# Kernel tuning notes

Hardware: AMD Instinct MI355X
Metric: run time of the kernel (lower is better)

Reference implementation:

```python
import jax, jax.numpy as jnp
import numpy as np

EMB = 1024
HEADS = 16
B, N = 2, 2048

def setup_inputs() -> dict:
    key = jax.random.key(0)
    ks = jax.random.split(key, 9)
    s = 1.0 / np.sqrt(EMB)
    return {
        "x": jax.random.normal(ks[0], (B, N, EMB), dtype=jnp.float32),
        "Wq": jax.random.normal(ks[1], (EMB, EMB), dtype=jnp.float32) * s,
        "bq": jax.random.normal(ks[2], (EMB,), dtype=jnp.float32) * 0.01,
        "Wk": jax.random.normal(ks[3], (EMB, EMB), dtype=jnp.float32) * s,
        "bk": jax.random.normal(ks[4], (EMB,), dtype=jnp.float32) * 0.01,
        "Wv": jax.random.normal(ks[5], (EMB, EMB), dtype=jnp.float32) * s,
        "bv": jax.random.normal(ks[6], (EMB,), dtype=jnp.float32) * 0.01,
        "Wo": jax.random.normal(ks[7], (EMB, EMB), dtype=jnp.float32) * s,
        "bo": jax.random.normal(ks[8], (EMB,), dtype=jnp.float32) * 0.01,
    }

def _split_heads(t):
    b, n, e = t.shape
    return t.reshape(b, n, HEADS, e // HEADS).transpose(0, 2, 1, 3)  # b h n d

def reference(x, Wq, bq, Wk, bk, Wv, bv, Wo, bo):
    q = _split_heads(x @ Wq + bq)
    k = _split_heads(x @ Wk + bk)
    v = _split_heads(x @ Wv + bv)
    # NOTE: original scales by sqrt(emb_size), not sqrt(head_dim)
    scaling = jnp.asarray(EMB, x.dtype) ** 0.5
    energy = jnp.einsum('bhqd,bhkd->bhqk', q, k)
    att = jax.nn.softmax(energy / scaling, axis=-1)
    out = jnp.einsum('bhqk,bhkd->bhqd', att, v)
    out = out.transpose(0, 2, 1, 3).reshape(x.shape[0], x.shape[1], EMB)
    return out @ Wo + bo
```

## Files before the change

### kernel.cpp

```cpp
#include <hip/hip_runtime.h>
#include <hip/hip_bf16.h>

typedef __bf16 bf16_t;
typedef bf16_t bf16x8 __attribute__((ext_vector_type(8)));
typedef float f32x4 __attribute__((ext_vector_type(4)));
typedef float f32x16 __attribute__((ext_vector_type(16)));

#define EMB 1024
#define HEADS 16
#define BATCH 2
#define SEQ 2048
#define HD 64
#define TOKENS (BATCH * SEQ)

__device__ __forceinline__ void gld16(bf16_t* lds_dst, const bf16_t* g_src) {
    __builtin_amdgcn_global_load_lds(
        (const __attribute__((address_space(1))) unsigned int*)g_src,
        (__attribute__((address_space(3))) unsigned int*)lds_dst, 16, 0, 0);
}

__device__ __forceinline__ unsigned cvt_pk_bf16(float lo, float hi) {
    unsigned r;
    asm("v_cvt_pk_bf16_f32 %0, %1, %2" : "=v"(r) : "v"(lo), "v"(hi));
    return r;
}

__device__ __forceinline__ float exp2_fast(float x) {
#if __has_builtin(__builtin_amdgcn_exp2f)
    return __builtin_amdgcn_exp2f(x);
#else
    return __expf(x * 0.69314718056f);
#endif
}

__global__ __launch_bounds__(256) void convert_x(const float* __restrict__ x,
                                                 bf16_t* __restrict__ xb) {
    size_t i = ((size_t)blockIdx.x * 256 + threadIdx.x) * 16;
    f32x4 v0 = *(const f32x4*)&x[i];
    f32x4 v1 = *(const f32x4*)&x[i + 4];
    f32x4 v2 = *(const f32x4*)&x[i + 8];
    f32x4 v3 = *(const f32x4*)&x[i + 12];
    bf16x8 o0, o1;
#pragma unroll
    for (int j = 0; j < 4; ++j) {
        o0[j] = (bf16_t)v0[j]; o0[4 + j] = (bf16_t)v1[j];
        o1[j] = (bf16_t)v2[j]; o1[4 + j] = (bf16_t)v3[j];
    }
    *(bf16x8*)&xb[i] = o0;
    *(bf16x8*)&xb[i + 8] = o1;
}

__global__ __launch_bounds__(256) void prep_w(
    const float* __restrict__ W0, const float* __restrict__ W1,
    const float* __restrict__ W2, const float* __restrict__ W3,
    bf16_t* __restrict__ T0, bf16_t* __restrict__ T1,
    bf16_t* __restrict__ T2, bf16_t* __restrict__ T3) {
    __shared__ __align__(16) bf16_t T[64][72];
    int z = blockIdx.z;
    const float* src = (z == 0) ? W0 : (z == 1) ? W1 : (z == 2) ? W2 : W3;
    bf16_t* dst = (z == 0) ? T0 : (z == 1) ? T1 : (z == 2) ? T2 : T3;
    int k0 = blockIdx.y * 64, n0 = blockIdx.x * 64;
    int r = threadIdx.x >> 2, c4 = (threadIdx.x & 3) * 16;
    f32x4 v[4];
#pragma unroll
    for (int q = 0; q < 4; ++q)
        v[q] = *(const f32x4*)&src[(size_t)(k0 + r) * 1024 + n0 + c4 + q * 4];
#pragma unroll
    for (int j = 0; j < 16; ++j) T[c4 + j][r] = (bf16_t)v[j >> 2][j & 3];
    __syncthreads();
    bf16x8 o0 = *(const bf16x8*)&T[r][c4];
    bf16x8 o1 = *(const bf16x8*)&T[r][c4 + 8];
    *(bf16x8*)&dst[(size_t)(n0 + r) * 1024 + k0 + c4] = o0;
    *(bf16x8*)&dst[(size_t)(n0 + r) * 1024 + k0 + c4 + 8] = o1;
}

__global__ __launch_bounds__(256) void vtrans(const bf16_t* __restrict__ V,
                                              bf16_t* __restrict__ Vt) {
    __shared__ __align__(16) bf16_t T[64][72];
    int bh = blockIdx.y, n0 = blockIdx.x * 64;
    int r = threadIdx.x >> 2, c4 = (threadIdx.x & 3) * 16;
    const bf16_t* src = &V[((size_t)bh * SEQ + n0 + r) * HD + c4];
    bf16x8 v0 = *(const bf16x8*)&src[0];
    bf16x8 v1 = *(const bf16x8*)&src[8];
#pragma unroll
    for (int j = 0; j < 8; ++j) { T[c4 + j][r] = v0[j]; T[c4 + 8 + j][r] = v1[j]; }
    __syncthreads();
    bf16x8 o0 = *(const bf16x8*)&T[r][c4];
    bf16x8 o1 = *(const bf16x8*)&T[r][c4 + 8];
    bf16_t* dst = &Vt[((size_t)bh * HD + r) * SEQ + n0 + c4];
    *(bf16x8*)&dst[0] = o0;
    *(bf16x8*)&dst[8] = o1;
}

template <typename TO>
__global__ __launch_bounds__(256) void gemm128(
    const bf16_t* __restrict__ A,
    const bf16_t* __restrict__ Wt0, const bf16_t* __restrict__ Wt1, const bf16_t* __restrict__ Wt2,
    const float* __restrict__ b0, const float* __restrict__ b1, const float* __restrict__ b2,
    TO* __restrict__ o0, TO* __restrict__ o1, TO* __restrict__ o2,
    int md0, int md1, int md2, float sc0, float sc1, float sc2) {
    __shared__ __align__(16) bf16_t As[2][128 * 32];
    __shared__ __align__(16) bf16_t Bs[2][128 * 32];

    const int tid = threadIdx.x, w = tid >> 6, lane = tid & 63;
    const int quad = lane >> 4, c = lane & 15;
    const int wm = (w >> 1) * 64, wn = (w & 1) * 64;

    const int nx = blockIdx.y & 7, ny = blockIdx.x * 4 + (blockIdx.y >> 3);
    const int m0 = ny * 128, n0 = nx * 128;

    const int z = blockIdx.z;
    const bf16_t* W = (z == 0) ? Wt0 : (z == 1) ? Wt1 : Wt2;
    const float* bias = (z == 0) ? b0 : (z == 1) ? b1 : b2;
    TO* out = (z == 0) ? o0 : (z == 1) ? o1 : o2;
    const int mode = (z == 0) ? md0 : (z == 1) ? md1 : md2;
    const float scale = (z == 0) ? sc0 : (z == 1) ? sc1 : sc2;

    f32x4 acc[4][4];
#pragma unroll
    for (int i = 0; i < 4; ++i)
#pragma unroll
        for (int j = 0; j < 4; ++j) acc[i][j] = (f32x4){0.f, 0.f, 0.f, 0.f};

    const int srow = lane >> 2, schunk = lane & 3;
    const bf16_t* Ag = A + (size_t)m0 * 1024;
    const bf16_t* Bg = W + (size_t)n0 * 1024;

    int gsrc[2], ldst[2];
#pragma unroll
    for (int s = 0; s < 2; ++s) {
        int rg = (w * 2 + s) * 16;
        gsrc[s] = (rg + srow) * 1024 + schunk * 8;
        ldst[s] = rg * 32;
    }

#pragma unroll
    for (int s = 0; s < 2; ++s) {
        gld16(&As[0][ldst[s]], &Ag[gsrc[s]]);
        gld16(&Bs[0][ldst[s]], &Bg[gsrc[s]]);
    }
    __syncthreads();

#define GEMM_STEP(TT, CUR)                                                     \
    {                                                                          \
        if ((TT) + 1 < 32) {                                                   \
            int kn = ((TT) + 1) * 32;                                          \
            _Pragma("unroll")                                                  \
            for (int s = 0; s < 2; ++s) {                                      \
                gld16(&As[(CUR) ^ 1][ldst[s]], &Ag[gsrc[s] + kn]);             \
                gld16(&Bs[(CUR) ^ 1][ldst[s]], &Bg[gsrc[s] + kn]);             \
            }                                                                  \
        }                                                                      \
        bf16x8 af[4], bfv[4];                                                  \
        _Pragma("unroll")                                                      \
        for (int t = 0; t < 4; ++t)                                            \
            af[t] = *(const bf16x8*)&As[CUR][(wm + t * 16 + c) * 32 + quad * 8]; \
        _Pragma("unroll")                                                      \
        for (int t = 0; t < 4; ++t)                                            \
            bfv[t] = *(const bf16x8*)&Bs[CUR][(wn + t * 16 + c) * 32 + quad * 8]; \
        __builtin_amdgcn_s_setprio(1);                                         \
        _Pragma("unroll")                                                      \
        for (int mt = 0; mt < 4; ++mt)                                         \
            _Pragma("unroll")                                                  \
            for (int nt = 0; nt < 4; ++nt)                                     \
                acc[mt][nt] = __builtin_amdgcn_mfma_f32_16x16x32_bf16(         \
                    af[mt], bfv[nt], acc[mt][nt], 0, 0, 0);                    \
        __builtin_amdgcn_s_setprio(0);                                         \
        __syncthreads();                                                       \
    }

    for (int t = 0; t < 32; t += 2) {
        GEMM_STEP(t, 0)
        GEMM_STEP(t + 1, 1)
    }
#undef GEMM_STEP

#pragma unroll
    for (int nt = 0; nt < 4; ++nt) {
        int col = n0 + wn + nt * 16 + c;
        float bv = bias[col];
#pragma unroll
        for (int mt = 0; mt < 4; ++mt)
#pragma unroll
            for (int r = 0; r < 4; ++r) {
                int row = m0 + wm + mt * 16 + quad * 4 + r;
                float v = (acc[mt][nt][r] + bv) * scale;
                size_t idx;
                if (mode == 0) {
                    idx = (size_t)row * 1024 + col;
                } else {
                    int bb = row >> 11, n = row & 2047;
                    int hh = col >> 6, d = col & 63;
                    idx = ((size_t)(bb * HEADS + hh) * SEQ + n) * HD + d;
                }
                out[idx] = (TO)v;
            }
    }
}

__global__ __launch_bounds__(256) void attn_kernel(
    const bf16_t* __restrict__ Q, const bf16_t* __restrict__ K,
    const bf16_t* __restrict__ Vt, bf16_t* __restrict__ O) {
    __shared__ __align__(16) bf16_t Qs[128 * 64];
    __shared__ __align__(16) bf16_t Ks[2][64 * 64];
    __shared__ __align__(16) bf16_t Vs[2][64 * 64];

    const int tid = threadIdx.x, w = tid >> 6, lane = tid & 63;
    const int hi = lane >> 5, lq = lane & 31;

    const int lin = blockIdx.x + (blockIdx.y << 4);
    const int xcd = lin & 7, slot = lin >> 3;
    const int bh = xcd + ((slot >> 4) << 3);
    const int q0 = (slot & 15) << 7;
    const int b = bh >> 4, h = bh & 15;

    const int srow8 = lane >> 3, sch = lane & 7;

    const bf16_t* Qg = Q + ((size_t)bh * SEQ + q0) * HD;
    const bf16_t* Kg0 = K + (size_t)bh * SEQ * HD;
    const bf16_t* Vg0 = Vt + (size_t)bh * HD * SEQ;

    int sl[2], sgK[2], sgV[2];
#pragma unroll
    for (int s = 0; s < 2; ++s) {
        int rg = (w * 2 + s) * 8;
        int row = rg + srow8;
        int g = sch ^ (row & 7);
        sl[s] = rg * 64;
        sgK[s] = row * 64 + g * 8;
        sgV[s] = row * SEQ + g * 8;
    }
    int rd[4];
#pragma unroll
    for (int dc = 0; dc < 4; ++dc)
        rd[dc] = lq * 64 + (((dc * 2 + hi) ^ (lq & 7)) * 8);

#pragma unroll
    for (int s = 0; s < 4; ++s) {
        int rg = (w * 4 + s) * 8;
        int row = rg + srow8;
        int g = sch ^ (row & 7);
        gld16(&Qs[rg * 64], &Qg[(size_t)row * 64 + g * 8]);
    }
#pragma unroll
    for (int s = 0; s < 2; ++s) {
        gld16(&Ks[0][sl[s]], &Kg0[sgK[s]]);
        gld16(&Vs[0][sl[s]], &Vg0[sgV[s]]);
    }
    __syncthreads();

    bf16x8 qf[4];
#pragma unroll
    for (int dc = 0; dc < 4; ++dc)
        qf[dc] = *(const bf16x8*)&Qs[w * 2048 + rd[dc]];

    f32x16 Oacc0, Oacc1;
#pragma unroll
    for (int r = 0; r < 16; ++r) { Oacc0[r] = 0.f; Oacc1[r] = 0.f; }
    float lp = 0.f;

    const bf16_t* KgN = Kg0 + 64 * HD;
    const bf16_t* VgN = Vg0 + 64;

#define ATTN_STEP(TT, CUR)                                                     \
    {                                                                          \
        if ((TT) + 1 < SEQ / 64) {                                             \
            _Pragma("unroll")                                                  \
            for (int s = 0; s < 2; ++s) {                                      \
                gld16(&Ks[(CUR) ^ 1][sl[s]], &KgN[sgK[s]]);                    \
                gld16(&Vs[(CUR) ^ 1][sl[s]], &VgN[sgV[s]]);                    \
            }                                                                  \
            KgN += 64 * HD; VgN += 64;                                         \
        }                                                                      \
        f32x16 St0, St1;                                                       \
        _Pragma("unroll")                                                      \
        for (int r = 0; r < 16; ++r) { St0[r] = 0.f; St1[r] = 0.f; }           \
        __builtin_amdgcn_s_setprio(1);                                         \
        _Pragma("unroll")                                                      \
        for (int dc = 0; dc < 4; ++dc) {                                       \
            bf16x8 k0 = *(const bf16x8*)&Ks[CUR][rd[dc]];                      \
            bf16x8 k1 = *(const bf16x8*)&Ks[CUR][rd[dc] + 2048];               \
            St0 = __builtin_amdgcn_mfma_f32_32x32x16_bf16(k0, qf[dc], St0, 0, 0, 0); \
            St1 = __builtin_amdgcn_mfma_f32_32x32x16_bf16(k1, qf[dc], St1, 0, 0, 0); \
        }                                                                      \
        __builtin_amdgcn_s_setprio(0);                                         \
        _Pragma("unroll")                                                      \
        for (int r = 0; r < 16; ++r) {                                         \
            St0[r] = exp2_fast(St0[r]); lp += St0[r];                          \
            St1[r] = exp2_fast(St1[r]); lp += St1[r];                          \
        }                                                                      \
        bf16x8 pf[4];                                                          \
        PACKFRAG(St0, 0, 0) PACKFRAG(St0, 1, 1)                                \
        PACKFRAG(St1, 0, 2) PACKFRAG(St1, 1, 3)                                \
        __builtin_amdgcn_s_setprio(1);                                         \
        _Pragma("unroll")                                                      \
        for (int f = 0; f < 4; ++f) {                                          \
            bf16x8 v0 = *(const bf16x8*)&Vs[CUR][rd[f]];                       \
            bf16x8 v1 = *(const bf16x8*)&Vs[CUR][rd[f] + 2048];                \
            Oacc0 = __builtin_amdgcn_mfma_f32_32x32x16_bf16(pf[f], v0, Oacc0, 0, 0, 0); \
            Oacc1 = __builtin_amdgcn_mfma_f32_32x32x16_bf16(pf[f], v1, Oacc1, 0, 0, 0); \
        }                                                                      \
        __builtin_amdgcn_s_setprio(0);                                         \
        __syncthreads();                                                       \
    }

#define PACKFRAG(SS, c2, dstIdx)                                               \
        {                                                                      \
            unsigned pa = cvt_pk_bf16(SS[8 * (c2) + 0], SS[8 * (c2) + 1]);     \
            unsigned pb = cvt_pk_bf16(SS[8 * (c2) + 4], SS[8 * (c2) + 5]);     \
            unsigned pc = cvt_pk_bf16(SS[8 * (c2) + 2], SS[8 * (c2) + 3]);     \
            unsigned pd = cvt_pk_bf16(SS[8 * (c2) + 6], SS[8 * (c2) + 7]);     \
            asm volatile("v_permlane32_swap_b32 %0, %1" : "+v"(pa), "+v"(pb)); \
            asm volatile("v_permlane32_swap_b32 %0, %1" : "+v"(pc), "+v"(pd)); \
            union { unsigned u[4]; bf16x8 v; } pu;                             \
            pu.u[0] = pa; pu.u[1] = pc; pu.u[2] = pb; pu.u[3] = pd;            \
            pf[dstIdx] = pu.v;                                                 \
        }

    for (int t = 0; t < SEQ / 64; t += 2) {
        ATTN_STEP(t, 0)
        ATTN_STEP(t + 1, 1)
    }
#undef ATTN_STEP
#undef PACKFRAG

    lp += __shfl_xor(lp, 32);
    float rl = 1.0f / lp;

#pragma unroll
    for (int r = 0; r < 16; ++r) {
        int q_loc = (r & 3) + 8 * (r >> 2) + 4 * hi;
        float rr = __shfl(rl, q_loc);
        int qrow = q0 + w * 32 + q_loc;
        size_t base = ((size_t)(b * SEQ + qrow)) * EMB + h * 64;
        O[base + lq] = (bf16_t)(Oacc0[r] * rr);
        O[base + 32 + lq] = (bf16_t)(Oacc1[r] * rr);
    }
}

extern "C" void kernel_launch(void* const* d_in, const int* in_sizes, int n_in,
                              void* d_out, int out_size, void* d_ws, size_t ws_size,
                              hipStream_t stream) {
    (void)in_sizes; (void)n_in; (void)out_size; (void)ws_size;
    const float* x  = (const float*)d_in[0];
    const float* Wq = (const float*)d_in[1];
    const float* bq = (const float*)d_in[2];
    const float* Wk = (const float*)d_in[3];
    const float* bk = (const float*)d_in[4];
    const float* Wv = (const float*)d_in[5];
    const float* bv = (const float*)d_in[6];
    const float* Wo = (const float*)d_in[7];
    const float* bo = (const float*)d_in[8];

    bf16_t* ws = (bf16_t*)d_ws;
    const size_t NELEM = (size_t)TOKENS * EMB;
    const size_t WELEM = (size_t)EMB * EMB;
    bf16_t* Qb  = ws;
    bf16_t* Kb  = ws + NELEM;
    bf16_t* Vb  = ws + 2 * NELEM;
    bf16_t* Ob  = ws + 3 * NELEM;
    bf16_t* xb  = ws + 4 * NELEM;
    bf16_t* Vtb = xb;
    bf16_t* Wt0 = ws + 5 * NELEM;
    bf16_t* Wt1 = Wt0 + WELEM;
    bf16_t* Wt2 = Wt0 + 2 * WELEM;
    bf16_t* Wt3 = Wt0 + 3 * WELEM;

    hipLaunchKernelGGL(convert_x, dim3(1024), dim3(256), 0, stream, x, xb);
    hipLaunchKernelGGL(prep_w, dim3(16, 16, 4), dim3(256), 0, stream,
                       Wq, Wk, Wv, Wo, Wt0, Wt1, Wt2, Wt3);
    hipLaunchKernelGGL((gemm128<bf16_t>), dim3(8, 32, 3), dim3(256), 0, stream,
                       xb, Wt0, Wt1, Wt2, bq, bk, bv, Qb, Kb, Vb,
                       1, 1, 1, 0.0450842204f, 1.0f, 1.0f);
    hipLaunchKernelGGL(vtrans, dim3(32, 32), dim3(256), 0, stream, Vb, Vtb);
    hipLaunchKernelGGL(attn_kernel, dim3(16, 32), dim3(256), 0, stream, Qb, Kb, Vtb, Ob);
    hipLaunchKernelGGL((gemm128<float>), dim3(8, 32, 1), dim3(256), 0, stream,
                       Ob, Wt3, Wt3, Wt3, bo, bo, bo,
                       (float*)d_out, (float*)d_out, (float*)d_out,
                       0, 0, 0, 1.0f, 1.0f, 1.0f);
}
```

Measured before the change: 215.7 us.

## Triple-buffer GEMM and attention loads, fuse V transpose into QKV epilogue

Both the projection GEMM and the attention kernel move from double to triple-buffered LDS staging. Each step waits on a vmcnt counter and issues a raw barrier, which replaces a full __syncthreads after every step and lets two tiles be in flight during compute. The QKV GEMM epilogue gains a mode that writes V directly in transposed head layout with packed 4-element stores, removing the separate vtrans kernel launch and its extra memory pass. The cost is more LDS per block, which may reduce occupancy, and hand-tuned waitcnt values whose correctness depends on the number of outstanding loads.

```diff
diff --git a/kernel.cpp b/kernel.cpp
--- a/kernel.cpp
+++ b/kernel.cpp
@@ -32,6 +32,9 @@
     return __expf(x * 0.69314718056f);
 #endif
 }
+
+#define WAITV(N) asm volatile("s_waitcnt vmcnt(" #N ")" ::: "memory")
+#define BAR() __builtin_amdgcn_s_barrier()
 
 __global__ __launch_bounds__(256) void convert_x(const float* __restrict__ x,
                                                  bf16_t* __restrict__ xb) {
@@ -74,24 +77,6 @@
     *(bf16x8*)&dst[(size_t)(n0 + r) * 1024 + k0 + c4 + 8] = o1;
 }
 
-__global__ __launch_bounds__(256) void vtrans(const bf16_t* __restrict__ V,
-                                              bf16_t* __restrict__ Vt) {
-    __shared__ __align__(16) bf16_t T[64][72];
-    int bh = blockIdx.y, n0 = blockIdx.x * 64;
-    int r = threadIdx.x >> 2, c4 = (threadIdx.x & 3) * 16;
-    const bf16_t* src = &V[((size_t)bh * SEQ + n0 + r) * HD + c4];
-    bf16x8 v0 = *(const bf16x8*)&src[0];
-    bf16x8 v1 = *(const bf16x8*)&src[8];
-#pragma unroll
-    for (int j = 0; j < 8; ++j) { T[c4 + j][r] = v0[j]; T[c4 + 8 + j][r] = v1[j]; }
-    __syncthreads();
-    bf16x8 o0 = *(const bf16x8*)&T[r][c4];
-    bf16x8 o1 = *(const bf16x8*)&T[r][c4 + 8];
-    bf16_t* dst = &Vt[((size_t)bh * HD + r) * SEQ + n0 + c4];
-    *(bf16x8*)&dst[0] = o0;
-    *(bf16x8*)&dst[8] = o1;
-}
-
 template <typename TO>
 __global__ __launch_bounds__(256) void gemm128(
     const bf16_t* __restrict__ A,
@@ -99,8 +84,8 @@
     const float* __restrict__ b0, const float* __restrict__ b1, const float* __restrict__ b2,
     TO* __restrict__ o0, TO* __restrict__ o1, TO* __restrict__ o2,
     int md0, int md1, int md2, float sc0, float sc1, float sc2) {
-    __shared__ __align__(16) bf16_t As[2][128 * 32];
-    __shared__ __align__(16) bf16_t Bs[2][128 * 32];
+    __shared__ __align__(16) bf16_t As[3][128 * 32];
+    __shared__ __align__(16) bf16_t Bs[3][128 * 32];
 
     const int tid = threadIdx.x, w = tid >> 6, lane = tid & 63;
     const int quad = lane >> 4, c = lane & 15;
@@ -139,25 +124,21 @@
         gld16(&As[0][ldst[s]], &Ag[gsrc[s]]);
         gld16(&Bs[0][ldst[s]], &Bg[gsrc[s]]);
     }
-    __syncthreads();
-
-#define GEMM_STEP(TT, CUR)                                                     \
+#pragma unroll
+    for (int s = 0; s < 2; ++s) {
+        gld16(&As[1][ldst[s]], &Ag[gsrc[s] + 32]);
+        gld16(&Bs[1][ldst[s]], &Bg[gsrc[s] + 32]);
+    }
+
+#define GFRAGS(CUR)                                                            \
     {                                                                          \
-        if ((TT) + 1 < 32) {                                                   \
-            int kn = ((TT) + 1) * 32;                                          \
-            _Pragma("unroll")                                                  \
-            for (int s = 0; s < 2; ++s) {                                      \
-                gld16(&As[(CUR) ^ 1][ldst[s]], &Ag[gsrc[s] + kn]);             \
-                gld16(&Bs[(CUR) ^ 1][ldst[s]], &Bg[gsrc[s] + kn]);             \
-            }                                                                  \
-        }                                                                      \
         bf16x8 af[4], bfv[4];                                                  \
         _Pragma("unroll")                                                      \
-        for (int t = 0; t < 4; ++t)                                            \
-            af[t] = *(const bf16x8*)&As[CUR][(wm + t * 16 + c) * 32 + quad * 8]; \
-        _Pragma("unroll")                                                      \
-        for (int t = 0; t < 4; ++t)                                            \
-            bfv[t] = *(const bf16x8*)&Bs[CUR][(wn + t * 16 + c) * 32 + quad * 8]; \
+        for (int t2 = 0; t2 < 4; ++t2)                                         \
+            af[t2] = *(const bf16x8*)&As[CUR][(wm + t2 * 16 + c) * 32 + quad * 8]; \
+        _Pragma("unroll")                                                      \
+        for (int t2 = 0; t2 < 4; ++t2)                                         \
+            bfv[t2] = *(const bf16x8*)&Bs[CUR][(wn + t2 * 16 + c) * 32 + quad * 8]; \
         __builtin_amdgcn_s_setprio(1);                                         \
         _Pragma("unroll")                                                      \
         for (int mt = 0; mt < 4; ++mt)                                         \
@@ -166,35 +147,64 @@
                 acc[mt][nt] = __builtin_amdgcn_mfma_f32_16x16x32_bf16(         \
                     af[mt], bfv[nt], acc[mt][nt], 0, 0, 0);                    \
         __builtin_amdgcn_s_setprio(0);                                         \
-        __syncthreads();                                                       \
-    }
-
-    for (int t = 0; t < 32; t += 2) {
-        GEMM_STEP(t, 0)
-        GEMM_STEP(t + 1, 1)
-    }
-#undef GEMM_STEP
-
+    }
+
+#define GSTEP(T, CUR)                                                          \
+    {                                                                          \
+        WAITV(4);                                                              \
+        BAR();                                                                 \
+        int kn = ((T) + 2) * 32;                                               \
+        _Pragma("unroll")                                                      \
+        for (int s = 0; s < 2; ++s) {                                          \
+            gld16(&As[((CUR) + 2) % 3][ldst[s]], &Ag[gsrc[s] + kn]);           \
+            gld16(&Bs[((CUR) + 2) % 3][ldst[s]], &Bg[gsrc[s] + kn]);           \
+        }                                                                      \
+        GFRAGS(CUR)                                                            \
+    }
+
+    for (int t = 0; t < 30; t += 3) {
+        GSTEP(t, 0)
+        GSTEP(t + 1, 1)
+        GSTEP(t + 2, 2)
+    }
+    WAITV(4); BAR(); GFRAGS(0)
+    WAITV(0); BAR(); GFRAGS(1)
+#undef GSTEP
+#undef GFRAGS
+
+    typedef TO TOx4 __attribute__((ext_vector_type(4)));
 #pragma unroll
     for (int nt = 0; nt < 4; ++nt) {
         int col = n0 + wn + nt * 16 + c;
         float bv = bias[col];
 #pragma unroll
-        for (int mt = 0; mt < 4; ++mt)
-#pragma unroll
-            for (int r = 0; r < 4; ++r) {
-                int row = m0 + wm + mt * 16 + quad * 4 + r;
-                float v = (acc[mt][nt][r] + bv) * scale;
-                size_t idx;
-                if (mode == 0) {
-                    idx = (size_t)row * 1024 + col;
-                } else {
-                    int bb = row >> 11, n = row & 2047;
-                    int hh = col >> 6, d = col & 63;
-                    idx = ((size_t)(bb * HEADS + hh) * SEQ + n) * HD + d;
+        for (int mt = 0; mt < 4; ++mt) {
+            if (mode == 2) {
+                int row = m0 + wm + mt * 16 + quad * 4;
+                int bb = row >> 11, n = row & 2047;
+                int hh = col >> 6, d = col & 63;
+                TOx4 pk;
+#pragma unroll
+                for (int r = 0; r < 4; ++r)
+                    pk[r] = (TO)((acc[mt][nt][r] + bv) * scale);
+                *(TOx4*)&out[((size_t)(bb * HEADS + hh) * HD + d) * SEQ + n] = pk;
+            } else {
+#pragma unroll
+                for (int r = 0; r < 4; ++r) {
+                    int row = m0 + wm + mt * 16 + quad * 4 + r;
+                    float v = (acc[mt][nt][r] + bv) * scale;
+                    size_t idx;
+                    if (mode == 0) {
+                        idx = (size_t)row * 1024 + col;
+                    } else {
+                        int bb = row >> 11, n = row & 2047;
+                        int hh = col >> 6, d = col & 63;
+                        idx = ((size_t)(bb * HEADS + hh) * SEQ + n) * HD + d;
+                    }
+                    out[idx] = (TO)v;
                 }
-                out[idx] = (TO)v;
             }
+        }
     }
 }
 
@@ -202,8 +212,8 @@
     const bf16_t* __restrict__ Q, const bf16_t* __restrict__ K,
     const bf16_t* __restrict__ Vt, bf16_t* __restrict__ O) {
     __shared__ __align__(16) bf16_t Qs[128 * 64];
-    __shared__ __align__(16) bf16_t Ks[2][64 * 64];
-    __shared__ __align__(16) bf16_t Vs[2][64 * 64];
+    __shared__ __align__(16) bf16_t Ks[3][64 * 64];
+    __shared__ __align__(16) bf16_t Vs[3][64 * 64];
 
     const int tid = threadIdx.x, w = tid >> 6, lane = tid & 63;
     const int hi = lane >> 5, lq = lane & 31;
@@ -247,8 +257,14 @@
         gld16(&Ks[0][sl[s]], &Kg0[sgK[s]]);
         gld16(&Vs[0][sl[s]], &Vg0[sgV[s]]);
     }
-    __syncthreads();
-
+#pragma unroll
+    for (int s = 0; s < 2; ++s) {
+        gld16(&Ks[1][sl[s]], &Kg0[64 * HD + sgK[s]]);
+        gld16(&Vs[1][sl[s]], &Vg0[64 + sgV[s]]);
+    }
+
+    WAITV(8);
+    BAR();
     bf16x8 qf[4];
 #pragma unroll
     for (int dc = 0; dc < 4; ++dc)
@@ -259,50 +275,8 @@
     for (int r = 0; r < 16; ++r) { Oacc0[r] = 0.f; Oacc1[r] = 0.f; }
     float lp = 0.f;
 
-    const bf16_t* KgN = Kg0 + 64 * HD;
-    const bf16_t* VgN = Vg0 + 64;
-
-#define ATTN_STEP(TT, CUR)                                                     \
-    {                                                                          \
-        if ((TT) + 1 < SEQ / 64) {                                             \
-            _Pragma("unroll")                                                  \
-            for (int s = 0; s < 2; ++s) {                                      \
-                gld16(&Ks[(CUR) ^ 1][sl[s]], &KgN[sgK[s]]);                    \
-                gld16(&Vs[(CUR) ^ 1][sl[s]], &VgN[sgV[s]]);                    \
-            }                                                                  \
-            KgN += 64 * HD; VgN += 64;                                         \
-        }                                                                      \
-        f32x16 St0, St1;                                                       \
-        _Pragma("unroll")                                                      \
-        for (int r = 0; r < 16; ++r) { St0[r] = 0.f; St1[r] = 0.f; }           \
-        __builtin_amdgcn_s_setprio(1);                                         \
-        _Pragma("unroll")                                                      \
-        for (int dc = 0; dc < 4; ++dc) {                                       \
-            bf16x8 k0 = *(const bf16x8*)&Ks[CUR][rd[dc]];                      \
-            bf16x8 k1 = *(const bf16x8*)&Ks[CUR][rd[dc] + 2048];               \
-            St0 = __builtin_amdgcn_mfma_f32_32x32x16_bf16(k0, qf[dc], St0, 0, 0, 0); \
-            St1 = __builtin_amdgcn_mfma_f32_32x32x16_bf16(k1, qf[dc], St1, 0, 0, 0); \
-        }                                                                      \
-        __builtin_amdgcn_s_setprio(0);                                         \
-        _Pragma("unroll")                                                      \
-        for (int r = 0; r < 16; ++r) {                                         \
-            St0[r] = exp2_fast(St0[r]); lp += St0[r];                          \
-            St1[r] = exp2_fast(St1[r]); lp += St1[r];                          \
-        }                                                                      \
-        bf16x8 pf[4];                                                          \
-        PACKFRAG(St0, 0, 0) PACKFRAG(St0, 1, 1)                                \
-        PACKFRAG(St1, 0, 2) PACKFRAG(St1, 1, 3)                                \
-        __builtin_amdgcn_s_setprio(1);                                         \
-        _Pragma("unroll")                                                      \
-        for (int f = 0; f < 4; ++f) {                                          \
-            bf16x8 v0 = *(const bf16x8*)&Vs[CUR][rd[f]];                       \
-            bf16x8 v1 = *(const bf16x8*)&Vs[CUR][rd[f] + 2048];                \
-            Oacc0 = __builtin_amdgcn_mfma_f32_32x32x16_bf16(pf[f], v0, Oacc0, 0, 0, 0); \
-            Oacc1 = __builtin_amdgcn_mfma_f32_32x32x16_bf16(pf[f], v1, Oacc1, 0, 0, 0); \
-        }                                                                      \
-        __builtin_amdgcn_s_setprio(0);                                         \
-        __syncthreads();                                                       \
-    }
+    const bf16_t* KgN = Kg0 + 2 * 64 * HD;
+    const bf16_t* VgN = Vg0 + 2 * 64;
 
 #define PACKFRAG(SS, c2, dstIdx)                                               \
         {                                                                      \
@@ -317,11 +291,59 @@
             pf[dstIdx] = pu.v;                                                 \
         }
 
-    for (int t = 0; t < SEQ / 64; t += 2) {
-        ATTN_STEP(t, 0)
-        ATTN_STEP(t + 1, 1)
-    }
-#undef ATTN_STEP
+#define ACORE(CUR)                                                             \
+    {                                                                          \
+        f32x16 St0, St1;                                                       \
+        _Pragma("unroll")                                                      \
+        for (int r = 0; r < 16; ++r) { St0[r] = 0.f; St1[r] = 0.f; }           \
+        __builtin_amdgcn_s_setprio(1);                                         \
+        _Pragma("unroll")                                                      \
+        for (int dc = 0; dc < 4; ++dc) {                                       \
+            bf16x8 k0 = *(const bf16x8*)&Ks[CUR][rd[dc]];                      \
+            bf16x8 k1 = *(const bf16x8*)&Ks[CUR][rd[dc] + 2048];               \
+            St0 = __builtin_amdgcn_mfma_f32_32x32x16_bf16(k0, qf[dc], St0, 0, 0, 0); \
+            St1 = __builtin_amdgcn_mfma_f32_32x32x16_bf16(k1, qf[dc], St1, 0, 0, 0); \
+        }                                                                      \
+        __builtin_amdgcn_s_setprio(0);                                         \
+        _Pragma("unroll")                                                      \
+        for (int r = 0; r < 16; ++r) {                                         \
+            St0[r] = exp2_fast(St0[r]); lp += St0[r];                          \
+            St1[r] = exp2_fast(St1[r]); lp += St1[r];                          \
+        }                                                                      \
+        bf16x8 pf[4];                                                          \
+        PACKFRAG(St0, 0, 0) PACKFRAG(St0, 1, 1)                                \
+        PACKFRAG(St1, 0, 2) PACKFRAG(St1, 1, 3)                                \
+        __builtin_amdgcn_s_setprio(1);                                         \
+        _Pragma("unroll")                                                      \
+        for (int f = 0; f < 4; ++f) {                                          \
+            bf16x8 v0 = *(const bf16x8*)&Vs[CUR][rd[f]];                       \
+            bf16x8 v1 = *(const bf16x8*)&Vs[CUR][rd[f] + 2048];                \
+            Oacc0 = __builtin_amdgcn_mfma_f32_32x32x16_bf16(pf[f], v0, Oacc0, 0, 0, 0); \
+            Oacc1 = __builtin_amdgcn_mfma_f32_32x32x16_bf16(pf[f], v1, Oacc1, 0, 0, 0); \
+        }                                                                      \
+        __builtin_amdgcn_s_setprio(0);                                         \
+    }
+
+#define ASTEP(CUR)                                                             \
+    {                                                                          \
+        WAITV(4);                                                              \
+        BAR();                                                                 \
+        _Pragma("unroll")                                                      \
+        for (int s = 0; s < 2; ++s) {                                          \
+            gld16(&Ks[((CUR) + 2) % 3][sl[s]], &KgN[sgK[s]]);                  \
+            gld16(&Vs[((CUR) + 2) % 3][sl[s]], &VgN[sgV[s]]);                  \
+        }                                                                      \
+        KgN += 64 * HD; VgN += 64;                                             \
+        ACORE(CUR)                                                             \
+    }
+
+    for (int t = 0; t < 30; t += 3) {
+        ASTEP(0) ASTEP(1) ASTEP(2)
+    }
+    WAITV(4); BAR(); ACORE(0)
+    WAITV(0); BAR(); ACORE(1)
+#undef ASTEP
+#undef ACORE
 #undef PACKFRAG
 
     lp += __shfl_xor(lp, 32);
@@ -357,10 +379,9 @@
     const size_t WELEM = (size_t)EMB * EMB;
     bf16_t* Qb  = ws;
     bf16_t* Kb  = ws + NELEM;
-    bf16_t* Vb  = ws + 2 * NELEM;
+    bf16_t* Vtb = ws + 2 * NELEM;
     bf16_t* Ob  = ws + 3 * NELEM;
     bf16_t* xb  = ws + 4 * NELEM;
-    bf16_t* Vtb = xb;
     bf16_t* Wt0 = ws + 5 * NELEM;
     bf16_t* Wt1 = Wt0 + WELEM;
     bf16_t* Wt2 = Wt0 + 2 * WELEM;
@@ -370,9 +391,8 @@
     hipLaunchKernelGGL(prep_w, dim3(16, 16, 4), dim3(256), 0, stream,
                        Wq, Wk, Wv, Wo, Wt0, Wt1, Wt2, Wt3);
     hipLaunchKernelGGL((gemm128<bf16_t>), dim3(8, 32, 3), dim3(256), 0, stream,
-                       xb, Wt0, Wt1, Wt2, bq, bk, bv, Qb, Kb, Vb,
-                       1, 1, 1, 0.0450842204f, 1.0f, 1.0f);
-    hipLaunchKernelGGL(vtrans, dim3(32, 32), dim3(256), 0, stream, Vb, Vtb);
+                       xb, Wt0, Wt1, Wt2, bq, bk, bv, Qb, Kb, Vtb,
+                       1, 1, 2, 0.0450842204f, 1.0f, 1.0f);
     hipLaunchKernelGGL(attn_kernel, dim3(16, 32), dim3(256), 0, stream, Qb, Kb, Vtb, Ob);
     hipLaunchKernelGGL((gemm128<float>), dim3(8, 32, 1), dim3(256), 0, stream,
                        Ob, Wt3, Wt3, Wt3, bo, bo, bo,
```

Result: faster. 209.1 us (-3.1%).
